# Optimization experiments

Hardware: AMD Instinct MI355X
Metric: run time of the kernel (lower is better)

## Reference

```python
import jax, jax.numpy as jnp
import numpy as np

M, N, H, C = 50000, 50000, 32, 128
K, GROUPS = 15, 8
CPG = C // GROUPS           # 16, channels per group
RADIUS, SIGMA, INF = 2.5, 1.0, 1.0e6
EPS = 1e-5                  # GroupNorm eps
NEG_SLOPE = 0.1             # LeakyReLU slope in alpha MLP


def setup_inputs() -> dict:
    key = jax.random.key(0)
    ks = jax.random.split(key, 12)
    q_pts = jax.random.normal(ks[0], (M, 3), jnp.float32) * 5.0
    s_pts = q_pts  # same-resolution layer: q == s
    s_feats = jax.random.normal(ks[1], (N, C), jnp.float32)
    neighb_inds = jax.random.randint(ks[2], (M, H), 0, N + 1)  # N = padding index
    # kernel points: center + 14 points in a sphere of given radius
    kp = jax.random.normal(ks[3], (K, 3), jnp.float32)
    kp = kp / (jnp.linalg.norm(kp, axis=1, keepdims=True) + 1e-9) * RADIUS * 0.66
    k_pts = kp.at[0].set(0.0)
    # alpha MLP: Linear(C->C) + LeakyReLU + Linear(C->K*CPG)
    W1 = jax.random.normal(ks[4], (C, C), jnp.float32) * np.sqrt(2.0 / C)
    b1 = jnp.zeros((C,), jnp.float32)
    W2 = jax.random.normal(ks[5], (C, K * CPG), jnp.float32) * np.sqrt(2.0 / C)
    b2 = jnp.zeros((K * CPG,), jnp.float32)
    gn_w = jnp.ones((K * CPG,), jnp.float32)
    gn_b = jnp.zeros((K * CPG,), jnp.float32)
    return {"q_pts": q_pts, "s_pts": s_pts, "s_feats": s_feats,
            "neighb_inds": neighb_inds, "k_pts": k_pts,
            "W1": W1, "b1": b1, "W2": W2, "b2": b2,
            "gn_w": gn_w, "gn_b": gn_b}


def reference(q_pts, s_pts, s_feats, k_pts, W1, b1, W2, b2, gn_w, gn_b, neighb_inds):
    m = q_pts.shape[0]
    # ---- neighbor geometry (no_grad in original) ----
    s_pts_pad = jnp.concatenate([s_pts, jnp.full((1, 3), INF, s_pts.dtype)], 0)
    neighbors = s_pts_pad[neighb_inds] - q_pts[:, None, :]          # (M,H,3)
    sq = jnp.sum((neighbors[:, :, None, :] - k_pts) ** 2, -1)       # (M,H,K)
    nn_sq = jnp.min(sq, -1)                                         # (M,H)
    nn_1nn = jnp.argmin(sq, -1)                                     # (M,H)
    infl = jnp.clip(1.0 - jnp.sqrt(nn_sq) / SIGMA, 0.0)             # linear influence
    # ---- neighbor features gather (padding row = zeros) ----
    feats_pad = jnp.concatenate([s_feats, jnp.zeros((1, C), s_feats.dtype)], 0)
    neighbor_feats = feats_pad[neighb_inds]                         # (M,H,C)
    # ---- dynamic weights from center features (q==s -> pooled = s_feats) ----
    pooled = s_feats
    h = pooled @ W1 + b1
    h = jnp.where(h >= 0, h, NEG_SLOPE * h)                         # LeakyReLU(0.1)
    cw = (h @ W2 + b2).reshape(m, K, CPG)                           # (M,K,CPG)
    # GroupNorm(K groups over K*CPG channels), stats over (points, CPG) per group
    mu = jnp.mean(cw, axis=(0, 2), keepdims=True)
    var = jnp.var(cw, axis=(0, 2), keepdims=True)
    cw = (cw - mu) * jax.lax.rsqrt(var + EPS)
    cw = cw * gn_w.reshape(1, K, CPG) + gn_b.reshape(1, K, CPG)
    # ---- gather weights at nearest kernel point, modulate by influence ----
    nw = jnp.take_along_axis(cw, nn_1nn[:, :, None], axis=1)        # (M,H,CPG)
    nw = nw * infl[:, :, None]                                      # weight_act = identity
    # ---- multiply and sum over neighbors ----
    nf = neighbor_feats.reshape(m, H, CPG, GROUPS)
    out = jnp.sum(nf * nw[:, :, :, None], axis=1)                   # (M,CPG,GROUPS)
    return out.reshape(m, C)
```

## Files before the change

### kernel.cpp

```cpp
#include <hip/hip_runtime.h>
#include <hip/hip_bf16.h>

#define Mpts 50000
#define Npts 50000
#define Hn 32
#define Cc 128
#define Kk 15
#define NCW 240

typedef __attribute__((ext_vector_type(8))) short short8;
typedef __attribute__((ext_vector_type(4))) float f32x4;
typedef __attribute__((ext_vector_type(2))) float f32x2;

__device__ inline ushort f2bf(float f) {
  __hip_bfloat16 h = __float2bfloat16(f);
  return *reinterpret_cast<ushort*>(&h);
}
__device__ inline float bf2f(ushort u) {
  return __uint_as_float(((uint)u) << 16);
}

__global__ __launch_bounds__(256) void k0_weights(
    const float* __restrict__ W1, const float* __restrict__ W2,
    ushort* __restrict__ W1t, ushort* __restrict__ W2t,
    ushort* __restrict__ sfb, float* __restrict__ stats)
{
  __shared__ ushort TT[240][66];
  const int t = threadIdx.x;
  const int b = blockIdx.x;
  if (b < 2) {
    const int k0 = b * 64;
#pragma unroll
    for (int i = 0; i < 32; ++i) {
      int e = t + i * 256;
      int r = e >> 7, c = e & 127;
      TT[c][r] = f2bf(W1[(size_t)(k0 + r) * Cc + c]);
    }
    __syncthreads();
    int n = t >> 1, half = t & 1;
    union { short8 v[4]; ushort u[32]; } pk;
#pragma unroll
    for (int i = 0; i < 32; ++i) pk.u[i] = TT[n][half * 32 + i];
#pragma unroll
    for (int q = 0; q < 4; ++q)
      *(short8*)(W1t + (size_t)n * Cc + k0 + half * 32 + q * 8) = pk.v[q];
  } else if (b < 4) {
    const int k0 = (b - 2) * 64;
    for (int i = 0; i < 60; ++i) {
      int e = t + i * 256;
      int r = e / 240, c = e % 240;
      TT[c][r] = f2bf(W2[(size_t)(k0 + r) * NCW + c]);
    }
    __syncthreads();
    if (t < 240) {
      union { short8 v[8]; ushort u[64]; } pk;
#pragma unroll
      for (int i = 0; i < 64; ++i) pk.u[i] = TT[t][i];
#pragma unroll
      for (int q = 0; q < 8; ++q)
        *(short8*)(W2t + (size_t)t * Cc + k0 + q * 8) = pk.v[q];
    }
  } else {
    if (t < 16) {
      short8 z = short8{0,0,0,0,0,0,0,0};
      *(short8*)(sfb + (size_t)Npts * Cc + t * 8) = z;
    }
    if (t < 128) {
      float4 z4 = make_float4(0.f, 0.f, 0.f, 0.f);
      *(float4*)(stats + t * 4) = z4;
    }
  }
}

__global__ __launch_bounds__(256, 2) void k1_mlp(
    const float* __restrict__ sfeat, const ushort* __restrict__ W1t,
    const float* __restrict__ b1, const ushort* __restrict__ W2t,
    const float* __restrict__ b2, ushort* __restrict__ sfb,
    ushort* __restrict__ cw, float* __restrict__ stats)
{
  __shared__ __align__(16) ushort shT[128 * 128];
  __shared__ float red[2][15][4];

  const int t = threadIdx.x;
  const int r0 = blockIdx.x * 128;
  const int wid = t >> 6, lane = t & 63;
  const int l16 = lane & 15, lq = lane >> 4;

  float4 fA[8], fB[8];
#pragma unroll
  for (int p = 0; p < 8; ++p) {
    int id = p * 256 + t;
    int r = id >> 4, c = id & 15;
    int g = r0 + r;
    fA[p] = make_float4(0.f, 0.f, 0.f, 0.f);
    fB[p] = make_float4(0.f, 0.f, 0.f, 0.f);
    if (g < Mpts) {
      const float* src = sfeat + (size_t)g * Cc + c * 8;
      fA[p] = *(const float4*)(src);
      fB[p] = *(const float4*)(src + 4);
    }
  }
#pragma unroll
  for (int p = 0; p < 8; ++p) {
    int id = p * 256 + t;
    int r = id >> 4, c = id & 15;
    int g = r0 + r;
    union { short8 s; ushort u[8]; } pk;
    pk.u[0] = f2bf(fA[p].x); pk.u[1] = f2bf(fA[p].y); pk.u[2] = f2bf(fA[p].z); pk.u[3] = f2bf(fA[p].w);
    pk.u[4] = f2bf(fB[p].x); pk.u[5] = f2bf(fB[p].y); pk.u[6] = f2bf(fB[p].z); pk.u[7] = f2bf(fB[p].w);
    if (g < Mpts) *(short8*)(sfb + (size_t)g * Cc + c * 8) = pk.s;
    int byte = ((r * 256) + c * 16) ^ ((r & 7) << 4);
    *(short8*)((char*)shT + byte) = pk.s;
  }
  __syncthreads();

  const int arow = wid * 32 + l16;
  const int axor = (arow & 7) << 4;

  f32x4 acc1[2][8];
#pragma unroll
  for (int rt = 0; rt < 2; ++rt)
#pragma unroll
    for (int nt = 0; nt < 8; ++nt) acc1[rt][nt] = f32x4{0.f, 0.f, 0.f, 0.f};
#pragma unroll
  for (int kt = 0; kt < 4; ++kt) {
    int off = (kt * 32 + lq * 8) * 2;
    short8 a0 = *(const short8*)((const char*)shT + (((arow)      * 256 + off) ^ axor));
    short8 a1 = *(const short8*)((const char*)shT + (((arow + 16) * 256 + off) ^ axor));
#pragma unroll
    for (int nt = 0; nt < 8; ++nt) {
      short8 b = *(const short8*)(W1t + (size_t)(nt * 16 + l16) * Cc + kt * 32 + lq * 8);
      acc1[0][nt] = __builtin_amdgcn_mfma_f32_16x16x32_bf16(a0, b, acc1[0][nt], 0, 0, 0);
      acc1[1][nt] = __builtin_amdgcn_mfma_f32_16x16x32_bf16(a1, b, acc1[1][nt], 0, 0, 0);
    }
  }
#pragma unroll
  for (int nt = 0; nt < 8; ++nt) {
    int col = nt * 16 + l16;
    float bias = b1[col];
#pragma unroll
    for (int rt = 0; rt < 2; ++rt)
#pragma unroll
      for (int reg = 0; reg < 4; ++reg) {
        float h = acc1[rt][nt][reg] + bias;
        h = h >= 0.f ? h : 0.1f * h;
        int row = wid * 32 + rt * 16 + lq * 4 + reg;
        int byte = ((row * 256) + col * 2) ^ ((row & 7) << 4);
        *(ushort*)((char*)shT + byte) = f2bf(h);
      }
  }

  float s[15], ss[15];
#pragma unroll
  for (int j = 0; j < 15; ++j) { s[j] = 0.f; ss[j] = 0.f; }
#pragma unroll
  for (int pass = 0; pass < 2; ++pass) {
    const int J0 = pass * 8, NJ = pass ? 7 : 8;
    f32x4 acc2[2][8];
#pragma unroll
    for (int rt = 0; rt < 2; ++rt)
#pragma unroll
      for (int j = 0; j < 8; ++j) acc2[rt][j] = f32x4{0.f, 0.f, 0.f, 0.f};
#pragma unroll
    for (int kt = 0; kt < 4; ++kt) {
      int off = (kt * 32 + lq * 8) * 2;
      short8 a0 = *(const short8*)((const char*)shT + (((arow)      * 256 + off) ^ axor));
      short8 a1 = *(const short8*)((const char*)shT + (((arow + 16) * 256 + off) ^ axor));
#pragma unroll
      for (int j = 0; j < NJ; ++j) {
        short8 b = *(const short8*)(W2t + (size_t)((J0 + j) * 16 + l16) * Cc + kt * 32 + lq * 8);
        acc2[0][j] = __builtin_amdgcn_mfma_f32_16x16x32_bf16(a0, b, acc2[0][j], 0, 0, 0);
        acc2[1][j] = __builtin_amdgcn_mfma_f32_16x16x32_bf16(a1, b, acc2[1][j], 0, 0, 0);
      }
    }
#pragma unroll
    for (int j = 0; j < NJ; ++j) {
      int col = (J0 + j) * 16 + l16;
      float bias = b2[col];
#pragma unroll
      for (int rt = 0; rt < 2; ++rt)
#pragma unroll
        for (int reg = 0; reg < 4; ++reg) {
          int grow = r0 + wid * 32 + rt * 16 + lq * 4 + reg;
          if (grow < Mpts) {
            float v = acc2[rt][j][reg] + bias;
            cw[(size_t)grow * NCW + col] = f2bf(v);
            s[J0 + j] += v; ss[J0 + j] += v * v;
          }
        }
    }
  }

#pragma unroll
  for (int j = 0; j < 15; ++j) {
    for (int off = 32; off > 0; off >>= 1) {
      s[j]  += __shfl_xor(s[j],  off);
      ss[j] += __shfl_xor(ss[j], off);
    }
  }
  if (lane == 0) {
#pragma unroll
    for (int j = 0; j < 15; ++j) { red[0][j][wid] = s[j]; red[1][j][wid] = ss[j]; }
  }
  __syncthreads();
  float* st = stats + (blockIdx.x & 7) * 64;
  if (t < 15) {
    float S = red[0][t][0] + red[0][t][1] + red[0][t][2] + red[0][t][3];
    atomicAdd(&st[t], S);
  } else if (t >= 32 && t < 47) {
    int j = t - 32;
    float SS = red[1][j][0] + red[1][j][1] + red[1][j][2] + red[1][j][3];
    atomicAdd(&st[32 + j], SS);
  }
}

__global__ __launch_bounds__(256) void k3_out(
    const float* __restrict__ q_pts, const float* __restrict__ s_pts,
    const ushort* __restrict__ sfb, const int* __restrict__ nb,
    const float* __restrict__ kp, const float* __restrict__ gn_w,
    const float* __restrict__ gn_b, const ushort* __restrict__ cw,
    const float* __restrict__ stats, float* __restrict__ out)
{
  __shared__ float kpt[3][15];
  __shared__ float mus[16], rss[16];
  __shared__ float Atab[240], Btab[240];
  __shared__ float wtab[4][32][17];
  const int t = threadIdx.x;

  if (t < 15) {
    float S = 0.f, SS = 0.f;
#pragma unroll
    for (int r = 0; r < 8; ++r) { S += stats[r * 64 + t]; SS += stats[r * 64 + 32 + t]; }
    const float inv = 1.0f / (16.0f * (float)Mpts);
    float mu = S * inv;
    float var = SS * inv - mu * mu;
    mus[t] = mu;
    rss[t] = rsqrtf(var + 1e-5f);
  } else if (t < 60) {
    kpt[(t - 15) % 3][(t - 15) / 3] = kp[t - 15];
  }
  __syncthreads();
  if (t < 240) {
    int g = t >> 4;
    float a = rss[g] * gn_w[t];
    Atab[t] = a;
    Btab[t] = gn_b[t] - mus[g] * a;
  }
  __syncthreads();

  const int wid = t >> 6, lane = t & 63;
  const int m = blockIdx.x * 4 + wid;

  int idx = Npts; int ksel = 0; float infl = 0.f;
  if (lane < Hn) {
    idx = nb[m * Hn + lane];
    if (idx > Npts) idx = Npts;
    float qx = q_pts[m * 3 + 0], qy = q_pts[m * 3 + 1], qz = q_pts[m * 3 + 2];
    float px, py, pz;
    if (idx < Npts) { px = s_pts[idx * 3 + 0]; py = s_pts[idx * 3 + 1]; pz = s_pts[idx * 3 + 2]; }
    else            { px = 1.0e6f; py = 1.0e6f; pz = 1.0e6f; }
    float nx = px - qx, ny = py - qy, nz = pz - qz;
    float best = 1e30f;
#pragma unroll
    for (int k = 0; k < Kk; ++k) {
      float dx = nx - kpt[0][k], dy = ny - kpt[1][k], dz = nz - kpt[2][k];
      float d = dx * dx + dy * dy + dz * dz;
      if (d < best) { best = d; ksel = k; }
    }
    infl = 1.f - sqrtf(best);
    infl = infl > 0.f ? infl : 0.f;
  }

  const int ch8 = lane & 15;
  const uint4* fb = (const uint4*)sfb;
  uint4 fv[8];
#pragma unroll
  for (int j = 0; j < 8; ++j) {
    int h = (lane >> 4) + 4 * j;
    int ih = __shfl(idx, h);
    fv[j] = fb[ih * 16 + ch8];
  }

  {
    int h = lane >> 1;
    int kh = __shfl(ksel, h);
    float wI = __shfl(infl, h);
    int c0 = (lane & 1) * 8;
    uint4 cwv = *(const uint4*)(cw + (size_t)m * NCW + kh * 16 + c0);
    const uint* cu = (const uint*)&cwv;
#pragma unroll
    for (int i = 0; i < 4; ++i) {
      uint u = cu[i];
      int jj = kh * 16 + c0 + 2 * i;
      float v0 = __uint_as_float(u << 16);
      float v1 = __uint_as_float(u & 0xffff0000u);
      wtab[wid][h][c0 + 2 * i]     = fmaf(v0, Atab[jj],     Btab[jj])     * wI;
      wtab[wid][h][c0 + 2 * i + 1] = fmaf(v1, Atab[jj + 1], Btab[jj + 1]) * wI;
    }
  }

  f32x2 acc0 = {0.f, 0.f}, acc1 = {0.f, 0.f}, acc2 = {0.f, 0.f}, acc3 = {0.f, 0.f};
#pragma unroll
  for (int j = 0; j < 8; ++j) {
    int h = (lane >> 4) + 4 * j;
    float w = wtab[wid][h][ch8];
    f32x2 w2 = {w, w};
    uint ux = fv[j].x, uy = fv[j].y, uz = fv[j].z, uw = fv[j].w;
    f32x2 p0 = {__uint_as_float(ux << 16), __uint_as_float(ux & 0xffff0000u)};
    f32x2 p1 = {__uint_as_float(uy << 16), __uint_as_float(uy & 0xffff0000u)};
    f32x2 p2 = {__uint_as_float(uz << 16), __uint_as_float(uz & 0xffff0000u)};
    f32x2 p3 = {__uint_as_float(uw << 16), __uint_as_float(uw & 0xffff0000u)};
    acc0 = __builtin_elementwise_fma(p0, w2, acc0);
    acc1 = __builtin_elementwise_fma(p1, w2, acc1);
    acc2 = __builtin_elementwise_fma(p2, w2, acc2);
    acc3 = __builtin_elementwise_fma(p3, w2, acc3);
  }
#pragma unroll
  for (int off = 16; off <= 32; off <<= 1) {
    acc0[0] += __shfl_xor(acc0[0], off); acc0[1] += __shfl_xor(acc0[1], off);
    acc1[0] += __shfl_xor(acc1[0], off); acc1[1] += __shfl_xor(acc1[1], off);
    acc2[0] += __shfl_xor(acc2[0], off); acc2[1] += __shfl_xor(acc2[1], off);
    acc3[0] += __shfl_xor(acc3[0], off); acc3[1] += __shfl_xor(acc3[1], off);
  }
  if (lane < 16) {
    float4 o0; o0.x = acc0[0]; o0.y = acc0[1]; o0.z = acc1[0]; o0.w = acc1[1];
    float4 o1; o1.x = acc2[0]; o1.y = acc2[1]; o1.z = acc3[0]; o1.w = acc3[1];
    float* op = out + (size_t)m * Cc + ch8 * 8;
    *(float4*)(op)     = o0;
    *(float4*)(op + 4) = o1;
  }
}

extern "C" void kernel_launch(void* const* d_in, const int* in_sizes, int n_in,
                              void* d_out, int out_size, void* d_ws, size_t ws_size,
                              hipStream_t stream) {
  const float* q_pts  = (const float*)d_in[0];
  const float* s_pts  = (const float*)d_in[1];
  const float* sfeat  = (const float*)d_in[2];
  const int*   nb     = (const int*)d_in[3];
  const float* kp     = (const float*)d_in[4];
  const float* W1     = (const float*)d_in[5];
  const float* b1     = (const float*)d_in[6];
  const float* W2     = (const float*)d_in[7];
  const float* b2     = (const float*)d_in[8];
  const float* gn_w   = (const float*)d_in[9];
  const float* gn_b   = (const float*)d_in[10];
  float* out   = (float*)d_out;

  char* wsb = (char*)d_ws;
  float*  stats = (float*)wsb;
  ushort* sfb   = (ushort*)(wsb + 4096);
  ushort* W1t   = (ushort*)(wsb + 4096 + 12800256);
  ushort* W2t   = (ushort*)(wsb + 4096 + 12800256 + 32768);
  ushort* cwb   = (ushort*)(wsb + 4096 + 12800256 + 32768 + 61440);

  k0_weights<<<5, 256, 0, stream>>>(W1, W2, W1t, W2t, sfb, stats);
  k1_mlp<<<(Mpts + 127) / 128, 256, 0, stream>>>(sfeat, W1t, b1, W2t, b2, sfb, cwb, stats);
  k3_out<<<Mpts / 4, 256, 0, stream>>>(q_pts, s_pts, sfb, nb, kp, gn_w, gn_b, cwb, stats, out);
}
```

Measured before the change: 114.6 us.

## Halve MLP tile rows and process two points per wave in output kernel

The MLP kernel now handles 64 rows per block (16 per wave), with a single 15-tile second GEMM pass and occupancy hint raised to 3. The output kernel gives each wave two query points, so all 64 lanes do neighbor geometry and two feature gathers are issued before the accumulation. The GroupNorm affine tables are padded to stride 17 to reduce LDS bank conflicts. The aim is better lane utilization and more memory-level parallelism, at the cost of more registers per thread and possibly less reuse of W1t/W2t per block.

```diff
diff --git a/kernel.cpp b/kernel.cpp
--- a/kernel.cpp
+++ b/kernel.cpp
@@ -15,9 +15,6 @@
 __device__ inline ushort f2bf(float f) {
   __hip_bfloat16 h = __float2bfloat16(f);
   return *reinterpret_cast<ushort*>(&h);
-}
-__device__ inline float bf2f(ushort u) {
-  return __uint_as_float(((uint)u) << 16);
 }
 
 __global__ __launch_bounds__(256) void k0_weights(
@@ -72,23 +69,23 @@
   }
 }
 
-__global__ __launch_bounds__(256, 2) void k1_mlp(
+__global__ __launch_bounds__(256, 3) void k1_mlp(
     const float* __restrict__ sfeat, const ushort* __restrict__ W1t,
     const float* __restrict__ b1, const ushort* __restrict__ W2t,
     const float* __restrict__ b2, ushort* __restrict__ sfb,
     ushort* __restrict__ cw, float* __restrict__ stats)
 {
-  __shared__ __align__(16) ushort shT[128 * 128];
+  __shared__ __align__(16) ushort shT[64 * 128];
   __shared__ float red[2][15][4];
 
   const int t = threadIdx.x;
-  const int r0 = blockIdx.x * 128;
+  const int r0 = blockIdx.x * 64;
   const int wid = t >> 6, lane = t & 63;
   const int l16 = lane & 15, lq = lane >> 4;
 
-  float4 fA[8], fB[8];
-#pragma unroll
-  for (int p = 0; p < 8; ++p) {
+  float4 fA[4], fB[4];
+#pragma unroll
+  for (int p = 0; p < 4; ++p) {
     int id = p * 256 + t;
     int r = id >> 4, c = id & 15;
     int g = r0 + r;
@@ -101,7 +98,7 @@
     }
   }
 #pragma unroll
-  for (int p = 0; p < 8; ++p) {
+  for (int p = 0; p < 4; ++p) {
     int id = p * 256 + t;
     int r = id >> 4, c = id & 15;
     int g = r0 + r;
@@ -114,24 +111,20 @@
   }
   __syncthreads();
 
-  const int arow = wid * 32 + l16;
+  const int arow = wid * 16 + l16;
   const int axor = (arow & 7) << 4;
 
-  f32x4 acc1[2][8];
-#pragma unroll
-  for (int rt = 0; rt < 2; ++rt)
-#pragma unroll
-    for (int nt = 0; nt < 8; ++nt) acc1[rt][nt] = f32x4{0.f, 0.f, 0.f, 0.f};
+  f32x4 acc1[8];
+#pragma unroll
+  for (int nt = 0; nt < 8; ++nt) acc1[nt] = f32x4{0.f, 0.f, 0.f, 0.f};
 #pragma unroll
   for (int kt = 0; kt < 4; ++kt) {
     int off = (kt * 32 + lq * 8) * 2;
-    short8 a0 = *(const short8*)((const char*)shT + (((arow)      * 256 + off) ^ axor));
-    short8 a1 = *(const short8*)((const char*)shT + (((arow + 16) * 256 + off) ^ axor));
+    short8 a = *(const short8*)((const char*)shT + ((arow * 256 + off) ^ axor));
 #pragma unroll
     for (int nt = 0; nt < 8; ++nt) {
       short8 b = *(const short8*)(W1t + (size_t)(nt * 16 + l16) * Cc + kt * 32 + lq * 8);
-      acc1[0][nt] = __builtin_amdgcn_mfma_f32_16x16x32_bf16(a0, b, acc1[0][nt], 0, 0, 0);
-      acc1[1][nt] = __builtin_amdgcn_mfma_f32_16x16x32_bf16(a1, b, acc1[1][nt], 0, 0, 0);
+      acc1[nt] = __builtin_amdgcn_mfma_f32_16x16x32_bf16(a, b, acc1[nt], 0, 0, 0);
     }
   }
 #pragma unroll
@@ -139,58 +132,46 @@
     int col = nt * 16 + l16;
     float bias = b1[col];
 #pragma unroll
-    for (int rt = 0; rt < 2; ++rt)
-#pragma unroll
-      for (int reg = 0; reg < 4; ++reg) {
-        float h = acc1[rt][nt][reg] + bias;
-        h = h >= 0.f ? h : 0.1f * h;
-        int row = wid * 32 + rt * 16 + lq * 4 + reg;
-        int byte = ((row * 256) + col * 2) ^ ((row & 7) << 4);
-        *(ushort*)((char*)shT + byte) = f2bf(h);
+    for (int reg = 0; reg < 4; ++reg) {
+      float h = acc1[nt][reg] + bias;
+      h = h >= 0.f ? h : 0.1f * h;
+      int row = wid * 16 + lq * 4 + reg;
+      int byte = ((row * 256) + col * 2) ^ ((row & 7) << 4);
+      *(ushort*)((char*)shT + byte) = f2bf(h);
+    }
+  }
+
+  f32x4 acc2[15];
+#pragma unroll
+  for (int j = 0; j < 15; ++j) acc2[j] = f32x4{0.f, 0.f, 0.f, 0.f};
+#pragma unroll
+  for (int kt = 0; kt < 4; ++kt) {
+    int off = (kt * 32 + lq * 8) * 2;
+    short8 a = *(const short8*)((const char*)shT + ((arow * 256 + off) ^ axor));
+#pragma unroll
+    for (int j = 0; j < 15; ++j) {
+      short8 b = *(const short8*)(W2t + (size_t)(j * 16 + l16) * Cc + kt * 32 + lq * 8);
+      acc2[j] = __builtin_amdgcn_mfma_f32_16x16x32_bf16(a, b, acc2[j], 0, 0, 0);
+    }
+  }
+
+  float s[15], ss[15];
+#pragma unroll
+  for (int j = 0; j < 15; ++j) { s[j] = 0.f; ss[j] = 0.f; }
+#pragma unroll
+  for (int j = 0; j < 15; ++j) {
+    int col = j * 16 + l16;
+    float bias = b2[col];
+#pragma unroll
+    for (int reg = 0; reg < 4; ++reg) {
+      int grow = r0 + wid * 16 + lq * 4 + reg;
+      if (grow < Mpts) {
+        float v = acc2[j][reg] + bias;
+        cw[(size_t)grow * NCW + col] = f2bf(v);
+        s[j] += v; ss[j] += v * v;
       }
-  }
-
-  float s[15], ss[15];
-#pragma unroll
-  for (int j = 0; j < 15; ++j) { s[j] = 0.f; ss[j] = 0.f; }
-#pragma unroll
-  for (int pass = 0; pass < 2; ++pass) {
-    const int J0 = pass * 8, NJ = pass ? 7 : 8;
-    f32x4 acc2[2][8];
-#pragma unroll
-    for (int rt = 0; rt < 2; ++rt)
-#pragma unroll
-      for (int j = 0; j < 8; ++j) acc2[rt][j] = f32x4{0.f, 0.f, 0.f, 0.f};
-#pragma unroll
-    for (int kt = 0; kt < 4; ++kt) {
-      int off = (kt * 32 + lq * 8) * 2;
-      short8 a0 = *(const short8*)((const char*)shT + (((arow)      * 256 + off) ^ axor));
-      short8 a1 = *(const short8*)((const char*)shT + (((arow + 16) * 256 + off) ^ axor));
-#pragma unroll
-      for (int j = 0; j < NJ; ++j) {
-        short8 b = *(const short8*)(W2t + (size_t)((J0 + j) * 16 + l16) * Cc + kt * 32 + lq * 8);
-        acc2[0][j] = __builtin_amdgcn_mfma_f32_16x16x32_bf16(a0, b, acc2[0][j], 0, 0, 0);
-        acc2[1][j] = __builtin_amdgcn_mfma_f32_16x16x32_bf16(a1, b, acc2[1][j], 0, 0, 0);
-      }
-    }
-#pragma unroll
-    for (int j = 0; j < NJ; ++j) {
-      int col = (J0 + j) * 16 + l16;
-      float bias = b2[col];
-#pragma unroll
-      for (int rt = 0; rt < 2; ++rt)
-#pragma unroll
-        for (int reg = 0; reg < 4; ++reg) {
-          int grow = r0 + wid * 32 + rt * 16 + lq * 4 + reg;
-          if (grow < Mpts) {
-            float v = acc2[rt][j][reg] + bias;
-            cw[(size_t)grow * NCW + col] = f2bf(v);
-            s[J0 + j] += v; ss[J0 + j] += v * v;
-          }
-        }
-    }
-  }
-
+    }
+  }
 #pragma unroll
   for (int j = 0; j < 15; ++j) {
     for (int off = 32; off > 0; off >>= 1) {
@@ -223,8 +204,8 @@
 {
   __shared__ float kpt[3][15];
   __shared__ float mus[16], rss[16];
-  __shared__ float Atab[240], Btab[240];
-  __shared__ float wtab[4][32][17];
+  __shared__ float Atab[255], Btab[255];
+  __shared__ float wtab[4][2][32][17];
   const int t = threadIdx.x;
 
   if (t < 15) {
@@ -240,22 +221,27 @@
     kpt[(t - 15) % 3][(t - 15) / 3] = kp[t - 15];
   }
   __syncthreads();
-  if (t < 240) {
-    int g = t >> 4;
-    float a = rss[g] * gn_w[t];
-    Atab[t] = a;
-    Btab[t] = gn_b[t] - mus[g] * a;
+  if (t < 255) {
+    int k = t / 17, c = t % 17;
+    if (c < 16) {
+      int j = k * 16 + c;
+      float a = rss[k] * gn_w[j];
+      Atab[t] = a;
+      Btab[t] = gn_b[j] - mus[k] * a;
+    }
   }
   __syncthreads();
 
   const int wid = t >> 6, lane = t & 63;
-  const int m = blockIdx.x * 4 + wid;
-
-  int idx = Npts; int ksel = 0; float infl = 0.f;
-  if (lane < Hn) {
-    idx = nb[m * Hn + lane];
+  const int mbase = blockIdx.x * 8 + wid * 2;
+
+  int idx; int ksel = 0; float infl;
+  {
+    const int mg = mbase + (lane >> 5);
+    const int hl = lane & 31;
+    idx = nb[mg * Hn + hl];
     if (idx > Npts) idx = Npts;
-    float qx = q_pts[m * 3 + 0], qy = q_pts[m * 3 + 1], qz = q_pts[m * 3 + 2];
+    float qx = q_pts[mg * 3 + 0], qy = q_pts[mg * 3 + 1], qz = q_pts[mg * 3 + 2];
     float px, py, pz;
     if (idx < Npts) { px = s_pts[idx * 3 + 0]; py = s_pts[idx * 3 + 1]; pz = s_pts[idx * 3 + 2]; }
     else            { px = 1.0e6f; py = 1.0e6f; pz = 1.0e6f; }
@@ -273,62 +259,76 @@
 
   const int ch8 = lane & 15;
   const uint4* fb = (const uint4*)sfb;
-  uint4 fv[8];
+  uint4 fv0[8], fv1[8];
 #pragma unroll
   for (int j = 0; j < 8; ++j) {
     int h = (lane >> 4) + 4 * j;
-    int ih = __shfl(idx, h);
-    fv[j] = fb[ih * 16 + ch8];
-  }
-
-  {
+    int ih0 = __shfl(idx, h);
+    fv0[j] = fb[ih0 * 16 + ch8];
+  }
+#pragma unroll
+  for (int j = 0; j < 8; ++j) {
+    int h = (lane >> 4) + 4 * j;
+    int ih1 = __shfl(idx, 32 + h);
+    fv1[j] = fb[ih1 * 16 + ch8];
+  }
+
+#pragma unroll
+  for (int p = 0; p < 2; ++p) {
     int h = lane >> 1;
-    int kh = __shfl(ksel, h);
-    float wI = __shfl(infl, h);
+    int kh = __shfl(ksel, p * 32 + h);
+    float wI = __shfl(infl, p * 32 + h);
     int c0 = (lane & 1) * 8;
-    uint4 cwv = *(const uint4*)(cw + (size_t)m * NCW + kh * 16 + c0);
+    uint4 cwv = *(const uint4*)(cw + (size_t)(mbase + p) * NCW + kh * 16 + c0);
     const uint* cu = (const uint*)&cwv;
 #pragma unroll
     for (int i = 0; i < 4; ++i) {
       uint u = cu[i];
-      int jj = kh * 16 + c0 + 2 * i;
+      int jj = kh * 17 + c0 + 2 * i;
       float v0 = __uint_as_float(u << 16);
       float v1 = __uint_as_float(u & 0xffff0000u);
-      wtab[wid][h][c0 + 2 * i]     = fmaf(v0, Atab[jj],     Btab[jj])     * wI;
-      wtab[wid][h][c0 + 2 * i + 1] = fmaf(v1, Atab[jj + 1], Btab[jj + 1]) * wI;
-    }
-  }
-
-  f32x2 acc0 = {0.f, 0.f}, acc1 = {0.f, 0.f}, acc2 = {0.f, 0.f}, acc3 = {0.f, 0.f};
-#pragma unroll
-  for (int j = 0; j < 8; ++j) {
-    int h = (lane >> 4) + 4 * j;
-    float w = wtab[wid][h][ch8];
-    f32x2 w2 = {w, w};
-    uint ux = fv[j].x, uy = fv[j].y, uz = fv[j].z, uw = fv[j].w;
-    f32x2 p0 = {__uint_as_float(ux << 16), __uint_as_float(ux & 0xffff0000u)};
-    f32x2 p1 = {__uint_as_float(uy << 16), __uint_as_float(uy & 0xffff0000u)};
-    f32x2 p2 = {__uint_as_float(uz << 16), __uint_as_float(uz & 0xffff0000u)};
-    f32x2 p3 = {__uint_as_float(uw << 16), __uint_as_float(uw & 0xffff0000u)};
-    acc0 = __builtin_elementwise_fma(p0, w2, acc0);
-    acc1 = __builtin_elementwise_fma(p1, w2, acc1);
-    acc2 = __builtin_elementwise_fma(p2, w2, acc2);
-    acc3 = __builtin_elementwise_fma(p3, w2, acc3);
-  }
-#pragma unroll
-  for (int off = 16; off <= 32; off <<= 1) {
-    acc0[0] += __shfl_xor(acc0[0], off); acc0[1] += __shfl_xor(acc0[1], off);
-    acc1[0] += __shfl_xor(acc1[0], off); acc1[1] += __shfl_xor(acc1[1], off);
-    acc2[0] += __shfl_xor(acc2[0], off); acc2[1] += __shfl_xor(acc2[1], off);
-    acc3[0] += __shfl_xor(acc3[0], off); acc3[1] += __shfl_xor(acc3[1], off);
-  }
-  if (lane < 16) {
-    float4 o0; o0.x = acc0[0]; o0.y = acc0[1]; o0.z = acc1[0]; o0.w = acc1[1];
-    float4 o1; o1.x = acc2[0]; o1.y = acc2[1]; o1.z = acc3[0]; o1.w = acc3[1];
-    float* op = out + (size_t)m * Cc + ch8 * 8;
-    *(float4*)(op)     = o0;
-    *(float4*)(op + 4) = o1;
-  }
+      wtab[wid][p][h][c0 + 2 * i]     = fmaf(v0, Atab[jj],     Btab[jj])     * wI;
+      wtab[wid][p][h][c0 + 2 * i + 1] = fmaf(v1, Atab[jj + 1], Btab[jj + 1]) * wI;
+    }
+  }
+
+#define K3_MAIN(FV, P)                                                         \
+  {                                                                            \
+    f32x2 acc0 = {0.f, 0.f}, acc1 = {0.f, 0.f}, acc2 = {0.f, 0.f}, acc3 = {0.f, 0.f}; \
+    _Pragma("unroll")                                                          \
+    for (int j = 0; j < 8; ++j) {                                              \
+      int h = (lane >> 4) + 4 * j;                                             \
+      float w = wtab[wid][P][h][ch8];                                          \
+      f32x2 w2 = {w, w};                                                       \
+      uint ux = FV[j].x, uy = FV[j].y, uz = FV[j].z, uw = FV[j].w;             \
+      f32x2 p0 = {__uint_as_float(ux << 16), __uint_as_float(ux & 0xffff0000u)}; \
+      f32x2 p1 = {__uint_as_float(uy << 16), __uint_as_float(uy & 0xffff0000u)}; \
+      f32x2 p2 = {__uint_as_float(uz << 16), __uint_as_float(uz & 0xffff0000u)}; \
+      f32x2 p3 = {__uint_as_float(uw << 16), __uint_as_float(uw & 0xffff0000u)}; \
+      acc0 = __builtin_elementwise_fma(p0, w2, acc0);                          \
+      acc1 = __builtin_elementwise_fma(p1, w2, acc1);                          \
+      acc2 = __builtin_elementwise_fma(p2, w2, acc2);                          \
+      acc3 = __builtin_elementwise_fma(p3, w2, acc3);                          \
+    }                                                                          \
+    _Pragma("unroll")                                                          \
+    for (int off = 16; off <= 32; off <<= 1) {                                 \
+      acc0[0] += __shfl_xor(acc0[0], off); acc0[1] += __shfl_xor(acc0[1], off); \
+      acc1[0] += __shfl_xor(acc1[0], off); acc1[1] += __shfl_xor(acc1[1], off); \
+      acc2[0] += __shfl_xor(acc2[0], off); acc2[1] += __shfl_xor(acc2[1], off); \
+      acc3[0] += __shfl_xor(acc3[0], off); acc3[1] += __shfl_xor(acc3[1], off); \
+    }                                                                          \
+    if (lane < 16) {                                                           \
+      float4 o0; o0.x = acc0[0]; o0.y = acc0[1]; o0.z = acc1[0]; o0.w = acc1[1]; \
+      float4 o1; o1.x = acc2[0]; o1.y = acc2[1]; o1.z = acc3[0]; o1.w = acc3[1]; \
+      float* op = out + (size_t)(mbase + P) * Cc + ch8 * 8;                    \
+      *(float4*)(op)     = o0;                                                 \
+      *(float4*)(op + 4) = o1;                                                 \
+    }                                                                          \
+  }
+
+  K3_MAIN(fv0, 0)
+  K3_MAIN(fv1, 1)
+#undef K3_MAIN
 }
 
 extern "C" void kernel_launch(void* const* d_in, const int* in_sizes, int n_in,
@@ -355,6 +355,6 @@
   ushort* cwb   = (ushort*)(wsb + 4096 + 12800256 + 32768 + 61440);
 
   k0_weights<<<5, 256, 0, stream>>>(W1, W2, W1t, W2t, sfb, stats);
-  k1_mlp<<<(Mpts + 127) / 128, 256, 0, stream>>>(sfeat, W1t, b1, W2t, b2, sfb, cwb, stats);
-  k3_out<<<Mpts / 4, 256, 0, stream>>>(q_pts, s_pts, sfb, nb, kp, gn_w, gn_b, cwb, stats, out);
-}
+  k1_mlp<<<(Mpts + 63) / 64, 256, 0, stream>>>(sfeat, W1t, b1, W2t, b2, sfb, cwb, stats);
+  k3_out<<<Mpts / 8, 256, 0, stream>>>(q_pts, s_pts, sfb, nb, kp, gn_w, gn_b, cwb, stats, out);
+}
```

Result: slower. 135.8 us (+18.6%).
